# Kernel optimization log

Hardware: AMD Instinct MI355X
Metric: run time of the kernel (lower is better)

## Reference

```python
import jax, jax.numpy as jnp
import numpy as np

B, S, D_IN, D_OUT, N_SENT = 32, 4096, 1024, 256, 64

def setup_inputs() -> dict:
    key = jax.random.key(0)
    k1, k2, k3 = jax.random.split(key, 3)
    enc_output = jax.random.normal(k1, (B, S, D_IN), dtype=jnp.float32)
    # xavier-normal init like the torch module
    W = jax.random.normal(k2, (D_IN, D_OUT), dtype=jnp.float32) * np.sqrt(2.0 / (D_IN + D_OUT))
    b = jnp.zeros((D_OUT,), dtype=jnp.float32)
    # sentence start positions: sorted, first CLS at position 0
    cls_pos = jnp.sort(jax.random.randint(k3, (B, N_SENT), 0, S - 1), axis=1)
    cls_pos = cls_pos.at[:, 0].set(0).astype(jnp.int32)
    # last SEP near the end of the sequence for every example
    last_sep = jnp.full((B,), S - 2, dtype=jnp.int32)
    return {"enc_output": enc_output, "W": W, "b": b,
            "max_num_sent": N_SENT, "cls_pos": cls_pos, "last_sep": last_sep}

def reference(enc_output, W, b, max_num_sent, cls_pos, last_sep):
    # linear projection: [B,S,D_IN] @ [D_IN,D_OUT] + b -> [B,S,D_OUT]
    x = jnp.einsum('bsd,do->bso', enc_output, W) + b
    seq_len = x.shape[1]
    # exclusive-prefix-sum trick: segment sum [a,b) = csum[b] - csum[a]
    csum = jnp.concatenate([jnp.zeros_like(x[:, :1]), jnp.cumsum(x, axis=1)], axis=1)  # [B,S+1,O]
    starts = cls_pos  # [B,N]
    ends = jnp.concatenate([cls_pos[:, 1:], (last_sep + 1)[:, None]], axis=1)  # [B,N]
    # torch semantics for the last segment: if idx2 == idx1, sum x[i, idx1:, :]
    last_end = jnp.where(ends[:, -1] > starts[:, -1], ends[:, -1], seq_len)
    ends = ends.at[:, -1].set(last_end)
    gather = lambda idx: jnp.take_along_axis(csum, idx[:, :, None].astype(jnp.int32), axis=1)
    segment_vecs = gather(ends) - gather(starts)  # [B, N, O]
    return jax.nn.log_softmax(segment_vecs, axis=-1)
```

## Files before the change

kernel.cpp:

```cpp
#include <hip/hip_runtime.h>
#include <math.h>

#define BATCH 32
#define SEQ   4096
#define DIN   1024
#define DOUT  256
#define NSENT 64

__global__ __launch_bounds__(256) void seg_sum_kernel(
    const float* __restrict__ enc,
    const int* __restrict__ cls_pos,
    const int* __restrict__ last_sep,
    float* __restrict__ seg) {
  const int row = blockIdx.x;
  const int bb  = row >> 6;
  const int n   = row & 63;

  const int start = cls_pos[bb * NSENT + n];
  int end;
  if (n < NSENT - 1) {
    end = cls_pos[bb * NSENT + n + 1];
  } else {
    end = last_sep[bb] + 1;
    if (end <= start) end = SEQ;
  }

  const int t = threadIdx.x;
  const float* base = enc + (size_t)bb * SEQ * DIN + t * 4;

  float4 acc = make_float4(0.f, 0.f, 0.f, 0.f);
  #pragma unroll 4
  for (int s = start; s < end; ++s) {
    const float4 v = *(const float4*)(base + (size_t)s * DIN);
    acc.x += v.x; acc.y += v.y; acc.z += v.z; acc.w += v.w;
  }
  *(float4*)(seg + (size_t)row * DIN + t * 4) = acc;
}

__global__ __launch_bounds__(256) void gemm_lsm_kernel(
    const float* __restrict__ seg,
    const float* __restrict__ W,
    const float* __restrict__ bias,
    const int* __restrict__ cls_pos,
    const int* __restrict__ last_sep,
    float* __restrict__ out) {
  const int t    = threadIdx.x;
  const int row0 = blockIdx.x * 8;

  float acc[8];
  #pragma unroll
  for (int r = 0; r < 8; ++r) acc[r] = 0.f;

  const float* s0 = seg + (size_t)row0 * DIN;

  for (int d = 0; d < DIN; d += 4) {
    const float w0 = W[(d + 0) * DOUT + t];
    const float w1 = W[(d + 1) * DOUT + t];
    const float w2 = W[(d + 2) * DOUT + t];
    const float w3 = W[(d + 3) * DOUT + t];
    #pragma unroll
    for (int r = 0; r < 8; ++r) {
      const float* sr = s0 + r * DIN + d;
      acc[r] = fmaf(sr[0], w0, acc[r]);
      acc[r] = fmaf(sr[1], w1, acc[r]);
      acc[r] = fmaf(sr[2], w2, acc[r]);
      acc[r] = fmaf(sr[3], w3, acc[r]);
    }
  }

  const float bt = bias[t];
  __shared__ float red[8][DOUT];
  __shared__ float m_s[8], l_s[8];

  #pragma unroll
  for (int r = 0; r < 8; ++r) {
    const int row = row0 + r;
    const int bb  = row >> 6;
    const int n   = row & 63;
    const int start = cls_pos[bb * NSENT + n];
    int end;
    if (n < NSENT - 1) {
      end = cls_pos[bb * NSENT + n + 1];
    } else {
      end = last_sep[bb] + 1;
      if (end <= start) end = SEQ;
    }
    int len = end - start;
    if (len < 0) len = 0;
    acc[r] += (float)len * bt;
    red[r][t] = acc[r];
  }
  __syncthreads();

  const int wave = t >> 6;
  const int lane = t & 63;
  for (int k = 0; k < 2; ++k) {
    const int r = wave * 2 + k;
    const float v0 = red[r][lane];
    const float v1 = red[r][lane + 64];
    const float v2 = red[r][lane + 128];
    const float v3 = red[r][lane + 192];
    float m = fmaxf(fmaxf(v0, v1), fmaxf(v2, v3));
    #pragma unroll
    for (int off = 32; off > 0; off >>= 1)
      m = fmaxf(m, __shfl_down(m, off));
    m = __shfl(m, 0);
    float ssum = expf(v0 - m) + expf(v1 - m) + expf(v2 - m) + expf(v3 - m);
    #pragma unroll
    for (int off = 32; off > 0; off >>= 1)
      ssum += __shfl_down(ssum, off);
    if (lane == 0) { m_s[r] = m; l_s[r] = logf(ssum); }
  }
  __syncthreads();

  #pragma unroll
  for (int r = 0; r < 8; ++r)
    out[(size_t)(row0 + r) * DOUT + t] = acc[r] - m_s[r] - l_s[r];
}

extern "C" void kernel_launch(void* const* d_in, const int* in_sizes, int n_in,
                              void* d_out, int out_size, void* d_ws, size_t ws_size,
                              hipStream_t stream) {
  const float* enc      = (const float*)d_in[0];
  const float* W        = (const float*)d_in[1];
  const float* bias     = (const float*)d_in[2];
  const int* cls_pos    = (const int*)d_in[4];
  const int* last_sep   = (const int*)d_in[5];
  float* out            = (float*)d_out;

  float* seg = (float*)d_ws;

  seg_sum_kernel<<<BATCH * NSENT, 256, 0, stream>>>(enc, cls_pos, last_sep, seg);
  gemm_lsm_kernel<<<(BATCH * NSENT) / 8, 256, 0, stream>>>(
      seg, W, bias, cls_pos, last_sep, out);
}
```

Baseline: 859.6 us.

## Split segment sums across multiple blocks and shrink GEMM row tile

Each segment's row sum is split across four blocks using a strided sequence walk, writing partial sums that a new combine kernel adds together. This raises memory-level parallelism for the bandwidth-heavy reduction. The GEMM/log-softmax kernel now handles 4 rows per block with vectorized float4 reads of segment rows, doubling the block count. The cost is an extra kernel launch and a workspace round-trip for the partials.

```diff
diff --git a/kernel.cpp b/kernel.cpp
--- a/kernel.cpp
+++ b/kernel.cpp
@@ -6,35 +6,61 @@
 #define DIN   1024
 #define DOUT  256
 #define NSENT 64
+#define NROWS (BATCH * NSENT)
+#define SPLIT 4
 
-__global__ __launch_bounds__(256) void seg_sum_kernel(
-    const float* __restrict__ enc,
-    const int* __restrict__ cls_pos,
-    const int* __restrict__ last_sep,
-    float* __restrict__ seg) {
-  const int row = blockIdx.x;
-  const int bb  = row >> 6;
-  const int n   = row & 63;
-
-  const int start = cls_pos[bb * NSENT + n];
-  int end;
+__device__ __forceinline__ void seg_bounds(const int* __restrict__ cls_pos,
+                                           const int* __restrict__ last_sep,
+                                           int row, int& start, int& end) {
+  const int bb = row >> 6;
+  const int n  = row & 63;
+  start = cls_pos[bb * NSENT + n];
   if (n < NSENT - 1) {
     end = cls_pos[bb * NSENT + n + 1];
   } else {
     end = last_sep[bb] + 1;
     if (end <= start) end = SEQ;
   }
+}
+
+__global__ __launch_bounds__(256) void seg_sum_part(
+    const float* __restrict__ enc,
+    const int* __restrict__ cls_pos,
+    const int* __restrict__ last_sep,
+    float* __restrict__ partial) {
+  const int blk = blockIdx.x;
+  const int row = blk >> 2;
+  const int j   = blk & (SPLIT - 1);
+  int start, end;
+  seg_bounds(cls_pos, last_sep, row, start, end);
 
   const int t = threadIdx.x;
-  const float* base = enc + (size_t)bb * SEQ * DIN + t * 4;
+  const float* base = enc + (size_t)(row >> 6) * SEQ * DIN + t * 4;
 
   float4 acc = make_float4(0.f, 0.f, 0.f, 0.f);
   #pragma unroll 4
-  for (int s = start; s < end; ++s) {
+  for (int s = start + j; s < end; s += SPLIT) {
     const float4 v = *(const float4*)(base + (size_t)s * DIN);
     acc.x += v.x; acc.y += v.y; acc.z += v.z; acc.w += v.w;
   }
-  *(float4*)(seg + (size_t)row * DIN + t * 4) = acc;
+  *(float4*)(partial + (size_t)blk * DIN + t * 4) = acc;
+}
+
+__global__ __launch_bounds__(256) void seg_combine(
+    const float* __restrict__ partial,
+    float* __restrict__ seg) {
+  const int row = blockIdx.x;
+  const int t   = threadIdx.x;
+  const float* p = partial + (size_t)row * SPLIT * DIN + t * 4;
+  float4 a = *(const float4*)(p);
+  const float4 b = *(const float4*)(p + DIN);
+  const float4 c = *(const float4*)(p + 2 * DIN);
+  const float4 d = *(const float4*)(p + 3 * DIN);
+  a.x += b.x + c.x + d.x;
+  a.y += b.y + c.y + d.y;
+  a.z += b.z + c.z + d.z;
+  a.w += b.w + c.w + d.w;
+  *(float4*)(seg + (size_t)row * DIN + t * 4) = a;
 }
 
 __global__ __launch_bounds__(256) void gemm_lsm_kernel(
@@ -45,46 +71,39 @@
     const int* __restrict__ last_sep,
     float* __restrict__ out) {
   const int t    = threadIdx.x;
-  const int row0 = blockIdx.x * 8;
+  const int row0 = blockIdx.x * 4;
 
-  float acc[8];
-  #pragma unroll
-  for (int r = 0; r < 8; ++r) acc[r] = 0.f;
-
+  float acc[4] = {0.f, 0.f, 0.f, 0.f};
   const float* s0 = seg + (size_t)row0 * DIN;
 
-  for (int d = 0; d < DIN; d += 4) {
-    const float w0 = W[(d + 0) * DOUT + t];
-    const float w1 = W[(d + 1) * DOUT + t];
-    const float w2 = W[(d + 2) * DOUT + t];
-    const float w3 = W[(d + 3) * DOUT + t];
+  for (int d = 0; d < DIN; d += 8) {
+    float w[8];
     #pragma unroll
-    for (int r = 0; r < 8; ++r) {
+    for (int k = 0; k < 8; ++k) w[k] = W[(d + k) * DOUT + t];
+    #pragma unroll
+    for (int r = 0; r < 4; ++r) {
       const float* sr = s0 + r * DIN + d;
-      acc[r] = fmaf(sr[0], w0, acc[r]);
-      acc[r] = fmaf(sr[1], w1, acc[r]);
-      acc[r] = fmaf(sr[2], w2, acc[r]);
-      acc[r] = fmaf(sr[3], w3, acc[r]);
+      const float4 sa = *(const float4*)(sr);
+      const float4 sb = *(const float4*)(sr + 4);
+      acc[r] = fmaf(sa.x, w[0], acc[r]);
+      acc[r] = fmaf(sa.y, w[1], acc[r]);
+      acc[r] = fmaf(sa.z, w[2], acc[r]);
+      acc[r] = fmaf(sa.w, w[3], acc[r]);
+      acc[r] = fmaf(sb.x, w[4], acc[r]);
+      acc[r] = fmaf(sb.y, w[5], acc[r]);
+      acc[r] = fmaf(sb.z, w[6], acc[r]);
+      acc[r] = fmaf(sb.w, w[7], acc[r]);
     }
   }
 
   const float bt = bias[t];
-  __shared__ float red[8][DOUT];
-  __shared__ float m_s[8], l_s[8];
+  __shared__ float red[4][DOUT];
+  __shared__ float m_s[4], l_s[4];
 
   #pragma unroll
-  for (int r = 0; r < 8; ++r) {
-    const int row = row0 + r;
-    const int bb  = row >> 6;
-    const int n   = row & 63;
-    const int start = cls_pos[bb * NSENT + n];
-    int end;
-    if (n < NSENT - 1) {
-      end = cls_pos[bb * NSENT + n + 1];
-    } else {
-      end = last_sep[bb] + 1;
-      if (end <= start) end = SEQ;
-    }
+  for (int r = 0; r < 4; ++r) {
+    int start, end;
+    seg_bounds(cls_pos, last_sep, row0 + r, start, end);
     int len = end - start;
     if (len < 0) len = 0;
     acc[r] += (float)len * bt;
@@ -94,8 +113,8 @@
 
   const int wave = t >> 6;
   const int lane = t & 63;
-  for (int k = 0; k < 2; ++k) {
-    const int r = wave * 2 + k;
+  {
+    const int r = wave;
     const float v0 = red[r][lane];
     const float v1 = red[r][lane + 64];
     const float v2 = red[r][lane + 128];
@@ -114,7 +133,7 @@
   __syncthreads();
 
   #pragma unroll
-  for (int r = 0; r < 8; ++r)
+  for (int r = 0; r < 4; ++r)
     out[(size_t)(row0 + r) * DOUT + t] = acc[r] - m_s[r] - l_s[r];
 }
 
@@ -128,9 +147,11 @@
   const int* last_sep   = (const int*)d_in[5];
   float* out            = (float*)d_out;
 
-  float* seg = (float*)d_ws;
+  float* partial = (float*)d_ws;
+  float* seg     = partial + (size_t)NROWS * SPLIT * DIN;
 
-  seg_sum_kernel<<<BATCH * NSENT, 256, 0, stream>>>(enc, cls_pos, last_sep, seg);
-  gemm_lsm_kernel<<<(BATCH * NSENT) / 8, 256, 0, stream>>>(
+  seg_sum_part<<<NROWS * SPLIT, 256, 0, stream>>>(enc, cls_pos, last_sep, partial);
+  seg_combine<<<NROWS, 256, 0, stream>>>(partial, seg);
+  gemm_lsm_kernel<<<NROWS / 4, 256, 0, stream>>>(
       seg, W, bias, cls_pos, last_sep, out);
 }
```

Result: faster. 760.8 us (-11.5%).
